# Kernel tuning notes

Hardware: AMD Instinct MI355X
Metric: run time of the kernel (lower is better)

Reference implementation:

```python
import jax, jax.numpy as jnp
import numpy as np

N_NODES = 50000
N_EDGES = 800000
IN_SIZE = 1024
EMB = 500


def setup_inputs() -> dict:
    key = jax.random.key(0)
    ks = jax.random.split(key, 9)
    x = jax.random.uniform(ks[0], (N_NODES, IN_SIZE), dtype=jnp.float32)
    edge_index = jax.random.randint(ks[1], (2, N_EDGES), 0, N_NODES, dtype=jnp.int32)
    edge_weight = jax.random.uniform(ks[2], (N_EDGES,), dtype=jnp.float32)
    s = 0.05
    wenc = jax.random.normal(ks[3], (EMB, IN_SIZE), dtype=jnp.float32) * s
    benc = jax.random.normal(ks[4], (EMB,), dtype=jnp.float32) * s
    wdec = jax.random.normal(ks[5], (IN_SIZE, EMB), dtype=jnp.float32) * s
    bdec = jax.random.normal(ks[6], (IN_SIZE,), dtype=jnp.float32) * s
    conv_weight = jax.random.normal(ks[7], (EMB, EMB), dtype=jnp.float32) * 0.1
    # lin.weight initialized N(0,0.1) + identity, per reset_parameters
    lin_weight = jax.random.normal(ks[8], (EMB, EMB), dtype=jnp.float32) * 0.1 + jnp.eye(EMB, dtype=jnp.float32)
    return {"x": x, "edge_index": edge_index, "edge_weight": edge_weight,
            "wenc": wenc, "benc": benc, "wdec": wdec, "bdec": bdec,
            "conv_weight": conv_weight, "lin_weight": lin_weight}


def reference(x, edge_index, edge_weight, wenc, benc, wdec, bdec, conv_weight, lin_weight):
    # encoder: h = sigmoid(x @ wenc^T + benc)          [N, EMB]
    h = jax.nn.sigmoid(x @ wenc.T + benc)
    # GraphConv (old PyG): neighbor transform then scatter-add to destinations
    h2 = h @ conv_weight                                # [N, EMB]
    src, dst = edge_index[0], edge_index[1]
    msgs = h2[src] * edge_weight[:, None]               # [E, EMB] gather + weight
    agg = jax.ops.segment_sum(msgs, dst, num_segments=x.shape[0])
    hout = agg + h @ lin_weight.T                       # root term via nn.Linear
    # decoder
    p = hout @ wdec.T + bdec                            # [N, IN_SIZE]
    return p
```

## Files before the change

### kernel.cpp

```cpp
#include <hip/hip_runtime.h>
#include <hip/hip_bf16.h>

typedef unsigned int u32;
typedef short bf16x8 __attribute__((ext_vector_type(8)));
typedef float floatx4 __attribute__((ext_vector_type(4)));

#define NNODES 50000
#define NEDGES 800000
#define INSZ   1024
#define EMB    500
#define EMBP   512

__device__ __forceinline__ short f2bf(float f) {
    u32 u = __builtin_bit_cast(u32, f);
    u32 r = u + 0x7FFFu + ((u >> 16) & 1u);
    return (short)(r >> 16);
}
__device__ __forceinline__ float bf2f(short h) {
    u32 u = ((u32)(unsigned short)h) << 16;
    return __builtin_bit_cast(float, u);
}

#define GLDS16(gp, lp) __builtin_amdgcn_global_load_lds( \
    (const __attribute__((address_space(1))) u32*)(gp),  \
    (__attribute__((address_space(3))) u32*)(lp), 16, 0, 0)

__global__ void pack_all(const float* __restrict__ wenc, const float* __restrict__ conv,
                         const float* __restrict__ lin,  const float* __restrict__ wdec,
                         short* __restrict__ wencP, short* __restrict__ Wmid,
                         short* __restrict__ wdecP) {
    int tid = blockIdx.x * 256 + threadIdx.x;
    {
        int m = tid >> 10, k = tid & 1023;
        wencP[tid] = (m < EMB) ? f2bf(wenc[m * INSZ + k]) : (short)0;
    }
    {
        int m = tid >> 10, k = tid & 1023;
        short v = 0;
        if (m < EMB) {
            if (k < EMBP) { if (k < EMB) v = f2bf(conv[k * EMB + m]); }
            else          { int kk = k - EMBP; if (kk < EMB) v = f2bf(lin[m * EMB + kk]); }
        }
        Wmid[tid] = v;
    }
    {
        int m = tid >> 9, k = tid & 511;
        wdecP[tid] = (k < EMB) ? f2bf(wdec[m * EMB + k]) : (short)0;
    }
}


__global__ __launch_bounds__(256)
void gemm_enc(const float* __restrict__ X, const short* __restrict__ Wp,
              const float* __restrict__ benc, short* __restrict__ H) {
    __shared__ short As[128 * 32];
    __shared__ short Bs[128 * 32];
    const int tid  = threadIdx.x;
    const int lane = tid & 63;
    const int wave = tid >> 6;
    const int wr   = (wave >> 1) * 64;
    const int wc   = (wave & 1) * 64;
    const int rowBase = blockIdx.y * 128;
    const int colBase = blockIdx.x * 128;

    floatx4 acc[4][4] = {};

    const int r0 = tid >> 2;
    const int c0 = (tid & 3) * 8;
    int ar0 = rowBase + r0;       if (ar0 >= NNODES) ar0 = NNODES - 1;
    int ar1 = rowBase + r0 + 64;  if (ar1 >= NNODES) ar1 = NNODES - 1;
    const float* xP0 = X + (size_t)ar0 * INSZ + c0;
    const float* xP1 = X + (size_t)ar1 * INSZ + c0;
    const short* bP0 = Wp + (size_t)(colBase + r0) * INSZ + c0;
    const short* bP1 = Wp + (size_t)(colBase + r0 + 64) * INSZ + c0;

    const int q8  = (lane >> 4) * 8;
    const int m16 = lane & 15;

    for (int k0 = 0; k0 < INSZ; k0 += 32) {
        {
            floatx4 fa = *(const floatx4*)(xP0 + k0);
            floatx4 fb = *(const floatx4*)(xP0 + k0 + 4);
            floatx4 fc = *(const floatx4*)(xP1 + k0);
            floatx4 fd = *(const floatx4*)(xP1 + k0 + 4);
            bf16x8 p0, p1;
#pragma unroll
            for (int j = 0; j < 4; ++j) {
                p0[j] = f2bf(fa[j]); p0[4 + j] = f2bf(fb[j]);
                p1[j] = f2bf(fc[j]); p1[4 + j] = f2bf(fd[j]);
            }
            *(bf16x8*)&As[tid * 8] = p0;
            *(bf16x8*)&As[2048 + tid * 8] = p1;
        }
        GLDS16(bP0 + k0, &Bs[tid * 8]);
        GLDS16(bP1 + k0, &Bs[2048 + tid * 8]);
        __syncthreads();

        bf16x8 af[4], bfr[4];
#pragma unroll
        for (int i = 0; i < 4; ++i) {
            af[i]  = *(const bf16x8*)&As[(wr + i * 16 + m16) * 32 + q8];
            bfr[i] = *(const bf16x8*)&Bs[(wc + i * 16 + m16) * 32 + q8];
        }
#pragma unroll
        for (int i = 0; i < 4; ++i)
#pragma unroll
            for (int j = 0; j < 4; ++j)
                acc[i][j] = __builtin_amdgcn_mfma_f32_16x16x32_bf16(af[i], bfr[j], acc[i][j], 0, 0, 0);
        __syncthreads();
    }

    const int rq = (lane >> 4) * 4;
#pragma unroll
    for (int i = 0; i < 4; ++i)
#pragma unroll
        for (int j = 0; j < 4; ++j)
#pragma unroll
            for (int reg = 0; reg < 4; ++reg) {
                int row = rowBase + wr + i * 16 + rq + reg;
                int col = colBase + wc + j * 16 + m16;
                if (row < NNODES) {
                    float b = (col < EMB) ? benc[col] : 0.f;
                    float v = 1.f / (1.f + __expf(-(acc[i][j][reg] + b)));
                    H[(size_t)row * EMBP + col] = f2bf(v);
                }
            }
}

__global__ __launch_bounds__(256)
void gemm_mid(const float* __restrict__ Agg, const short* __restrict__ H,
              const short* __restrict__ Wm, short* __restrict__ Hout) {
    __shared__ short As[128 * 32];
    __shared__ short Bs[128 * 32];
    const int tid  = threadIdx.x;
    const int lane = tid & 63;
    const int wave = tid >> 6;
    const int wr   = (wave >> 1) * 64;
    const int wc   = (wave & 1) * 64;
    const int rowBase = blockIdx.y * 128;
    const int colBase = blockIdx.x * 128;

    floatx4 acc[4][4] = {};

    const int r0 = tid >> 2;
    const int c0 = (tid & 3) * 8;
    int ar0 = rowBase + r0;       if (ar0 >= NNODES) ar0 = NNODES - 1;
    int ar1 = rowBase + r0 + 64;  if (ar1 >= NNODES) ar1 = NNODES - 1;
    const float* agP0 = Agg + (size_t)ar0 * EMBP + c0;
    const float* agP1 = Agg + (size_t)ar1 * EMBP + c0;
    const short* hP0  = H + (size_t)ar0 * EMBP + c0;
    const short* hP1  = H + (size_t)ar1 * EMBP + c0;
    const short* wP0  = Wm + (size_t)(colBase + r0) * 1024 + c0;
    const short* wP1  = Wm + (size_t)(colBase + r0 + 64) * 1024 + c0;

    const int q8  = (lane >> 4) * 8;
    const int m16 = lane & 15;

    for (int k0 = 0; k0 < 1024; k0 += 32) {
        if (k0 < 512) {
            floatx4 fa = *(const floatx4*)(agP0 + k0);
            floatx4 fb = *(const floatx4*)(agP0 + k0 + 4);
            floatx4 fc = *(const floatx4*)(agP1 + k0);
            floatx4 fd = *(const floatx4*)(agP1 + k0 + 4);
            bf16x8 p0, p1;
#pragma unroll
            for (int j = 0; j < 4; ++j) {
                p0[j] = f2bf(fa[j]); p0[4 + j] = f2bf(fb[j]);
                p1[j] = f2bf(fc[j]); p1[4 + j] = f2bf(fd[j]);
            }
            *(bf16x8*)&As[tid * 8] = p0;
            *(bf16x8*)&As[2048 + tid * 8] = p1;
        } else {
            GLDS16(hP0 + (k0 - 512), &As[tid * 8]);
            GLDS16(hP1 + (k0 - 512), &As[2048 + tid * 8]);
        }
        GLDS16(wP0 + k0, &Bs[tid * 8]);
        GLDS16(wP1 + k0, &Bs[2048 + tid * 8]);
        __syncthreads();

        bf16x8 af[4], bfr[4];
#pragma unroll
        for (int i = 0; i < 4; ++i) {
            af[i]  = *(const bf16x8*)&As[(wr + i * 16 + m16) * 32 + q8];
            bfr[i] = *(const bf16x8*)&Bs[(wc + i * 16 + m16) * 32 + q8];
        }
#pragma unroll
        for (int i = 0; i < 4; ++i)
#pragma unroll
            for (int j = 0; j < 4; ++j)
                acc[i][j] = __builtin_amdgcn_mfma_f32_16x16x32_bf16(af[i], bfr[j], acc[i][j], 0, 0, 0);
        __syncthreads();
    }

    const int rq = (lane >> 4) * 4;
#pragma unroll
    for (int i = 0; i < 4; ++i)
#pragma unroll
        for (int j = 0; j < 4; ++j)
#pragma unroll
            for (int reg = 0; reg < 4; ++reg) {
                int row = rowBase + wr + i * 16 + rq + reg;
                int col = colBase + wc + j * 16 + m16;
                if (row < NNODES)
                    Hout[(size_t)row * EMBP + col] = f2bf(acc[i][j][reg]);
            }
}

__global__ __launch_bounds__(256)
void gemm_dec(const short* __restrict__ Hout, const short* __restrict__ Wd,
              const float* __restrict__ bdec, float* __restrict__ Out) {
    __shared__ short As[128 * 32];
    __shared__ short Bs[128 * 32];
    const int tid  = threadIdx.x;
    const int lane = tid & 63;
    const int wave = tid >> 6;
    const int wr   = (wave >> 1) * 64;
    const int wc   = (wave & 1) * 64;
    const int rowBase = blockIdx.y * 128;
    const int colBase = blockIdx.x * 128;

    floatx4 acc[4][4] = {};

    const int r0 = tid >> 2;
    const int c0 = (tid & 3) * 8;
    int ar0 = rowBase + r0;       if (ar0 >= NNODES) ar0 = NNODES - 1;
    int ar1 = rowBase + r0 + 64;  if (ar1 >= NNODES) ar1 = NNODES - 1;
    const short* aP0 = Hout + (size_t)ar0 * EMBP + c0;
    const short* aP1 = Hout + (size_t)ar1 * EMBP + c0;
    const short* bP0 = Wd + (size_t)(colBase + r0) * EMBP + c0;
    const short* bP1 = Wd + (size_t)(colBase + r0 + 64) * EMBP + c0;

    const int q8  = (lane >> 4) * 8;
    const int m16 = lane & 15;

    for (int k0 = 0; k0 < EMBP; k0 += 32) {
        GLDS16(aP0 + k0, &As[tid * 8]);
        GLDS16(aP1 + k0, &As[2048 + tid * 8]);
        GLDS16(bP0 + k0, &Bs[tid * 8]);
        GLDS16(bP1 + k0, &Bs[2048 + tid * 8]);
        __syncthreads();

        bf16x8 af[4], bfr[4];
#pragma unroll
        for (int i = 0; i < 4; ++i) {
            af[i]  = *(const bf16x8*)&As[(wr + i * 16 + m16) * 32 + q8];
            bfr[i] = *(const bf16x8*)&Bs[(wc + i * 16 + m16) * 32 + q8];
        }
#pragma unroll
        for (int i = 0; i < 4; ++i)
#pragma unroll
            for (int j = 0; j < 4; ++j)
                acc[i][j] = __builtin_amdgcn_mfma_f32_16x16x32_bf16(af[i], bfr[j], acc[i][j], 0, 0, 0);
        __syncthreads();
    }

    const int rq = (lane >> 4) * 4;
#pragma unroll
    for (int i = 0; i < 4; ++i)
#pragma unroll
        for (int j = 0; j < 4; ++j)
#pragma unroll
            for (int reg = 0; reg < 4; ++reg) {
                int row = rowBase + wr + i * 16 + rq + reg;
                int col = colBase + wc + j * 16 + m16;
                if (row < NNODES)
                    Out[(size_t)row * INSZ + col] = acc[i][j][reg] + bdec[col];
            }
}


__global__ __launch_bounds__(256)
void count_edges(const int* __restrict__ dst, int* __restrict__ counts) {
    int e = blockIdx.x * 256 + threadIdx.x;
    atomicAdd(&counts[dst[e]], 1);
}

__global__ __launch_bounds__(1024)
void scan_counts(const int* __restrict__ counts, int* __restrict__ rowPtr,
                 int* __restrict__ cursor) {
    __shared__ int wsum[16];
    __shared__ int sbase;
    const int t = threadIdx.x;
    const int lane = t & 63;
    const int wv = t >> 6;
    if (t == 0) sbase = 0;
    for (int chunk = 0; chunk < 50176; chunk += 1024) {
        int i = chunk + t;
        int c = (i < NNODES) ? counts[i] : 0;
        int v = c;
#pragma unroll
        for (int off = 1; off < 64; off <<= 1) {
            int u = __shfl_up(v, off, 64);
            if (lane >= off) v += u;
        }
        if (lane == 63) wsum[wv] = v;
        __syncthreads();
        int woff = 0, total = 0;
#pragma unroll
        for (int w = 0; w < 16; ++w) {
            int s = wsum[w];
            if (w < wv) woff += s;
            total += s;
        }
        int base = sbase;
        __syncthreads();
        if (i < NNODES) {
            int p = base + woff + v - c;
            rowPtr[i] = p;
            cursor[i] = p;
        }
        if (t == 0) sbase = base + total;
        __syncthreads();
    }
}

__global__ __launch_bounds__(256)
void fill_csr(const int* __restrict__ src, const int* __restrict__ dst,
              const float* __restrict__ ew, int* __restrict__ cursor,
              int* __restrict__ csrSrc, float* __restrict__ csrW) {
    int e = blockIdx.x * 256 + threadIdx.x;
    int d = dst[e];
    int p = atomicAdd(&cursor[d], 1);
    csrSrc[p] = src[e];
    csrW[p]   = ew[e];
}

__global__ __launch_bounds__(256)
void aggregate(const short* __restrict__ H, const int* __restrict__ rowPtr,
               const int* __restrict__ counts, const int* __restrict__ csrSrc,
               const float* __restrict__ csrW, float* __restrict__ agg) {
    const int n    = blockIdx.x * 4 + (threadIdx.x >> 6);
    const int lane = threadIdx.x & 63;
    const int beg  = rowPtr[n];
    const int cnt  = counts[n];
    const short* hb = H + lane * 8;

    float acc[8] = {0.f, 0.f, 0.f, 0.f, 0.f, 0.f, 0.f, 0.f};
    int i = 0;
    for (; i + 2 <= cnt; i += 2) {
        int   s0 = csrSrc[beg + i];
        int   s1 = csrSrc[beg + i + 1];
        float w0 = csrW[beg + i];
        float w1 = csrW[beg + i + 1];
        bf16x8 v0 = *(const bf16x8*)(hb + (size_t)s0 * EMBP);
        bf16x8 v1 = *(const bf16x8*)(hb + (size_t)s1 * EMBP);
#pragma unroll
        for (int j = 0; j < 8; ++j)
            acc[j] += w0 * bf2f(v0[j]) + w1 * bf2f(v1[j]);
    }
    if (i < cnt) {
        int   s0 = csrSrc[beg + i];
        float w0 = csrW[beg + i];
        bf16x8 v0 = *(const bf16x8*)(hb + (size_t)s0 * EMBP);
#pragma unroll
        for (int j = 0; j < 8; ++j)
            acc[j] += w0 * bf2f(v0[j]);
    }

    floatx4 o0, o1;
#pragma unroll
    for (int j = 0; j < 4; ++j) { o0[j] = acc[j]; o1[j] = acc[4 + j]; }
    float* ap = agg + (size_t)n * EMBP + lane * 8;
    *(floatx4*)ap       = o0;
    *(floatx4*)(ap + 4) = o1;
}

extern "C" void kernel_launch(void* const* d_in, const int* in_sizes, int n_in,
                              void* d_out, int out_size, void* d_ws, size_t ws_size,
                              hipStream_t stream) {
    const float* x    = (const float*)d_in[0];
    const int*   ei   = (const int*)d_in[1];
    const float* ew   = (const float*)d_in[2];
    const float* wenc = (const float*)d_in[3];
    const float* benc = (const float*)d_in[4];
    const float* wdec = (const float*)d_in[5];
    const float* bdec = (const float*)d_in[6];
    const float* conv = (const float*)d_in[7];
    const float* lin  = (const float*)d_in[8];
    float* out = (float*)d_out;

    char* ws = (char*)d_ws;
    short* wencP = (short*)(ws);
    short* Wmid  = (short*)(ws + 1048576);
    short* wdecP = (short*)(ws + 2097152);
    short* h     = (short*)(ws + 3145728);
    short* hout  = (short*)(ws + 3145728 + 51200000);

    float* agg = (float*)d_out;

    char* scratch = (char*)d_out + 102400000;
    int*   counts = (int*)scratch;
    int*   rowPtr = counts + NNODES;
    int*   cursor = rowPtr + NNODES;
    int*   csrSrc = cursor + NNODES;
    float* csrW   = (float*)(csrSrc + NEDGES);

    hipMemsetAsync(counts, 0, (size_t)NNODES * 4, stream);

    dim3 blk(256);
    pack_all<<<2048, blk, 0, stream>>>(wenc, conv, lin, wdec, wencP, Wmid, wdecP);

    int rowTiles = (NNODES + 127) / 128;

    gemm_enc<<<dim3(EMBP / 128, rowTiles), blk, 0, stream>>>(x, wencP, benc, h);

    count_edges<<<NEDGES / 256, blk, 0, stream>>>(ei + NEDGES, counts);
    scan_counts<<<1, 1024, 0, stream>>>(counts, rowPtr, cursor);
    fill_csr<<<NEDGES / 256, blk, 0, stream>>>(ei, ei + NEDGES, ew, cursor, csrSrc, csrW);

    aggregate<<<NNODES / 4, blk, 0, stream>>>(h, rowPtr, counts, csrSrc, csrW, agg);

    gemm_mid<<<dim3(EMBP / 128, rowTiles), blk, 0, stream>>>(agg, h, Wmid, hout);

    gemm_dec<<<dim3(INSZ / 128, rowTiles), blk, 0, stream>>>(hout, wdecP, bdec, out);
}
```

Baseline: 957.8 us.

## Pre-convert X to bf16, double-buffer GEMMs, XCD swizzle, bf16 aggregation output

A separate kernel converts X to bf16 in scratch output memory, so the encoder GEMM can load A tiles asynchronously with global_load_lds. All three GEMMs now double-buffer LDS and prefetch the next K tile while computing the current one, and their block indices are remapped across XCDs. The aggregation is unrolled to four edges and writes bf16 instead of fp32, which halves its write traffic and lets gemm_mid load it directly. The trade-off is an extra full pass over X and reuse of the output buffer as scratch, with the counts memset moved after the encoder GEMM because that region is now overwritten.

```diff
diff --git a/kernel.cpp b/kernel.cpp
--- a/kernel.cpp
+++ b/kernel.cpp
@@ -24,6 +24,12 @@
 #define GLDS16(gp, lp) __builtin_amdgcn_global_load_lds( \
     (const __attribute__((address_space(1))) u32*)(gp),  \
     (__attribute__((address_space(3))) u32*)(lp), 16, 0, 0)
+
+__device__ __forceinline__ u32 xcd_swz(u32 orig, u32 q, u32 r) {
+    u32 xcd = orig & 7u, seq = orig >> 3;
+    u32 base = (xcd < r) ? xcd * (q + 1u) : r * (q + 1u) + (xcd - r) * q;
+    return base + seq;
+}
 
 __global__ void pack_all(const float* __restrict__ wenc, const float* __restrict__ conv,
                          const float* __restrict__ lin,  const float* __restrict__ wdec,
@@ -49,19 +55,31 @@
     }
 }
 
-
-__global__ __launch_bounds__(256)
-void gemm_enc(const float* __restrict__ X, const short* __restrict__ Wp,
+__global__ __launch_bounds__(256)
+void conv_x(const float* __restrict__ X, short* __restrict__ Xb) {
+    size_t base = ((size_t)blockIdx.x * 256 + threadIdx.x) * 8;
+    floatx4 f0 = *(const floatx4*)(X + base);
+    floatx4 f1 = *(const floatx4*)(X + base + 4);
+    bf16x8 p;
+#pragma unroll
+    for (int j = 0; j < 4; ++j) { p[j] = f2bf(f0[j]); p[4 + j] = f2bf(f1[j]); }
+    *(bf16x8*)(Xb + base) = p;
+}
+
+
+__global__ __launch_bounds__(256)
+void gemm_enc(const short* __restrict__ Xb, const short* __restrict__ Wp,
               const float* __restrict__ benc, short* __restrict__ H) {
-    __shared__ short As[128 * 32];
-    __shared__ short Bs[128 * 32];
+    __shared__ short As[2][128 * 32];
+    __shared__ short Bs[2][128 * 32];
     const int tid  = threadIdx.x;
     const int lane = tid & 63;
     const int wave = tid >> 6;
     const int wr   = (wave >> 1) * 64;
     const int wc   = (wave & 1) * 64;
-    const int rowBase = blockIdx.y * 128;
-    const int colBase = blockIdx.x * 128;
+    const u32 swz  = xcd_swz(blockIdx.y * 4 + blockIdx.x, 195, 4);
+    const int rowBase = (int)(swz >> 2) * 128;
+    const int colBase = (int)(swz & 3) * 128;
 
     floatx4 acc[4][4] = {};
 
@@ -69,38 +87,30 @@
     const int c0 = (tid & 3) * 8;
     int ar0 = rowBase + r0;       if (ar0 >= NNODES) ar0 = NNODES - 1;
     int ar1 = rowBase + r0 + 64;  if (ar1 >= NNODES) ar1 = NNODES - 1;
-    const float* xP0 = X + (size_t)ar0 * INSZ + c0;
-    const float* xP1 = X + (size_t)ar1 * INSZ + c0;
+    const short* aP0 = Xb + (size_t)ar0 * INSZ + c0;
+    const short* aP1 = Xb + (size_t)ar1 * INSZ + c0;
     const short* bP0 = Wp + (size_t)(colBase + r0) * INSZ + c0;
     const short* bP1 = Wp + (size_t)(colBase + r0 + 64) * INSZ + c0;
 
     const int q8  = (lane >> 4) * 8;
     const int m16 = lane & 15;
 
-    for (int k0 = 0; k0 < INSZ; k0 += 32) {
-        {
-            floatx4 fa = *(const floatx4*)(xP0 + k0);
-            floatx4 fb = *(const floatx4*)(xP0 + k0 + 4);
-            floatx4 fc = *(const floatx4*)(xP1 + k0);
-            floatx4 fd = *(const floatx4*)(xP1 + k0 + 4);
-            bf16x8 p0, p1;
-#pragma unroll
-            for (int j = 0; j < 4; ++j) {
-                p0[j] = f2bf(fa[j]); p0[4 + j] = f2bf(fb[j]);
-                p1[j] = f2bf(fc[j]); p1[4 + j] = f2bf(fd[j]);
-            }
-            *(bf16x8*)&As[tid * 8] = p0;
-            *(bf16x8*)&As[2048 + tid * 8] = p1;
-        }
-        GLDS16(bP0 + k0, &Bs[tid * 8]);
-        GLDS16(bP1 + k0, &Bs[2048 + tid * 8]);
-        __syncthreads();
-
+#define STAGE_E(buf, k0)                                   \
+    GLDS16(aP0 + (k0), &As[buf][tid * 8]);                 \
+    GLDS16(aP1 + (k0), &As[buf][2048 + tid * 8]);          \
+    GLDS16(bP0 + (k0), &Bs[buf][tid * 8]);                 \
+    GLDS16(bP1 + (k0), &Bs[buf][2048 + tid * 8]);
+
+    STAGE_E(0, 0);
+    __syncthreads();
+    int cur = 0;
+    for (int t = 0; t < 32; ++t) {
+        if (t + 1 < 32) { STAGE_E(cur ^ 1, (t + 1) * 32); }
         bf16x8 af[4], bfr[4];
 #pragma unroll
         for (int i = 0; i < 4; ++i) {
-            af[i]  = *(const bf16x8*)&As[(wr + i * 16 + m16) * 32 + q8];
-            bfr[i] = *(const bf16x8*)&Bs[(wc + i * 16 + m16) * 32 + q8];
+            af[i]  = *(const bf16x8*)&As[cur][(wr + i * 16 + m16) * 32 + q8];
+            bfr[i] = *(const bf16x8*)&Bs[cur][(wc + i * 16 + m16) * 32 + q8];
         }
 #pragma unroll
         for (int i = 0; i < 4; ++i)
@@ -108,7 +118,9 @@
             for (int j = 0; j < 4; ++j)
                 acc[i][j] = __builtin_amdgcn_mfma_f32_16x16x32_bf16(af[i], bfr[j], acc[i][j], 0, 0, 0);
         __syncthreads();
-    }
+        cur ^= 1;
+    }
+#undef STAGE_E
 
     const int rq = (lane >> 4) * 4;
 #pragma unroll
@@ -128,17 +140,18 @@
 }
 
 __global__ __launch_bounds__(256)
-void gemm_mid(const float* __restrict__ Agg, const short* __restrict__ H,
+void gemm_mid(const short* __restrict__ AggB, const short* __restrict__ H,
               const short* __restrict__ Wm, short* __restrict__ Hout) {
-    __shared__ short As[128 * 32];
-    __shared__ short Bs[128 * 32];
+    __shared__ short As[2][128 * 32];
+    __shared__ short Bs[2][128 * 32];
     const int tid  = threadIdx.x;
     const int lane = tid & 63;
     const int wave = tid >> 6;
     const int wr   = (wave >> 1) * 64;
     const int wc   = (wave & 1) * 64;
-    const int rowBase = blockIdx.y * 128;
-    const int colBase = blockIdx.x * 128;
+    const u32 swz  = xcd_swz(blockIdx.y * 4 + blockIdx.x, 195, 4);
+    const int rowBase = (int)(swz >> 2) * 128;
+    const int colBase = (int)(swz & 3) * 128;
 
     floatx4 acc[4][4] = {};
 
@@ -146,8 +159,8 @@
     const int c0 = (tid & 3) * 8;
     int ar0 = rowBase + r0;       if (ar0 >= NNODES) ar0 = NNODES - 1;
     int ar1 = rowBase + r0 + 64;  if (ar1 >= NNODES) ar1 = NNODES - 1;
-    const float* agP0 = Agg + (size_t)ar0 * EMBP + c0;
-    const float* agP1 = Agg + (size_t)ar1 * EMBP + c0;
+    const short* agP0 = AggB + (size_t)ar0 * EMBP + c0;
+    const short* agP1 = AggB + (size_t)ar1 * EMBP + c0;
     const short* hP0  = H + (size_t)ar0 * EMBP + c0;
     const short* hP1  = H + (size_t)ar1 * EMBP + c0;
     const short* wP0  = Wm + (size_t)(colBase + r0) * 1024 + c0;
@@ -156,33 +169,27 @@
     const int q8  = (lane >> 4) * 8;
     const int m16 = lane & 15;
 
-    for (int k0 = 0; k0 < 1024; k0 += 32) {
-        if (k0 < 512) {
-            floatx4 fa = *(const floatx4*)(agP0 + k0);
-            floatx4 fb = *(const floatx4*)(agP0 + k0 + 4);
-            floatx4 fc = *(const floatx4*)(agP1 + k0);
-            floatx4 fd = *(const floatx4*)(agP1 + k0 + 4);
-            bf16x8 p0, p1;
-#pragma unroll
-            for (int j = 0; j < 4; ++j) {
-                p0[j] = f2bf(fa[j]); p0[4 + j] = f2bf(fb[j]);
-                p1[j] = f2bf(fc[j]); p1[4 + j] = f2bf(fd[j]);
-            }
-            *(bf16x8*)&As[tid * 8] = p0;
-            *(bf16x8*)&As[2048 + tid * 8] = p1;
-        } else {
-            GLDS16(hP0 + (k0 - 512), &As[tid * 8]);
-            GLDS16(hP1 + (k0 - 512), &As[2048 + tid * 8]);
-        }
-        GLDS16(wP0 + k0, &Bs[tid * 8]);
-        GLDS16(wP1 + k0, &Bs[2048 + tid * 8]);
-        __syncthreads();
-
+#define STAGE_M(buf, k0)                                              \
+    if ((k0) < 512) {                                                 \
+        GLDS16(agP0 + (k0), &As[buf][tid * 8]);                       \
+        GLDS16(agP1 + (k0), &As[buf][2048 + tid * 8]);                \
+    } else {                                                          \
+        GLDS16(hP0 + ((k0) - 512), &As[buf][tid * 8]);                \
+        GLDS16(hP1 + ((k0) - 512), &As[buf][2048 + tid * 8]);         \
+    }                                                                 \
+    GLDS16(wP0 + (k0), &Bs[buf][tid * 8]);                            \
+    GLDS16(wP1 + (k0), &Bs[buf][2048 + tid * 8]);
+
+    STAGE_M(0, 0);
+    __syncthreads();
+    int cur = 0;
+    for (int t = 0; t < 32; ++t) {
+        if (t + 1 < 32) { STAGE_M(cur ^ 1, (t + 1) * 32); }
         bf16x8 af[4], bfr[4];
 #pragma unroll
         for (int i = 0; i < 4; ++i) {
-            af[i]  = *(const bf16x8*)&As[(wr + i * 16 + m16) * 32 + q8];
-            bfr[i] = *(const bf16x8*)&Bs[(wc + i * 16 + m16) * 32 + q8];
+            af[i]  = *(const bf16x8*)&As[cur][(wr + i * 16 + m16) * 32 + q8];
+            bfr[i] = *(const bf16x8*)&Bs[cur][(wc + i * 16 + m16) * 32 + q8];
         }
 #pragma unroll
         for (int i = 0; i < 4; ++i)
@@ -190,7 +197,9 @@
             for (int j = 0; j < 4; ++j)
                 acc[i][j] = __builtin_amdgcn_mfma_f32_16x16x32_bf16(af[i], bfr[j], acc[i][j], 0, 0, 0);
         __syncthreads();
-    }
+        cur ^= 1;
+    }
+#undef STAGE_M
 
     const int rq = (lane >> 4) * 4;
 #pragma unroll
@@ -209,15 +218,16 @@
 __global__ __launch_bounds__(256)
 void gemm_dec(const short* __restrict__ Hout, const short* __restrict__ Wd,
               const float* __restrict__ bdec, float* __restrict__ Out) {
-    __shared__ short As[128 * 32];
-    __shared__ short Bs[128 * 32];
+    __shared__ short As[2][128 * 32];
+    __shared__ short Bs[2][128 * 32];
     const int tid  = threadIdx.x;
     const int lane = tid & 63;
     const int wave = tid >> 6;
     const int wr   = (wave >> 1) * 64;
     const int wc   = (wave & 1) * 64;
-    const int rowBase = blockIdx.y * 128;
-    const int colBase = blockIdx.x * 128;
+    const u32 swz  = xcd_swz(blockIdx.y * 8 + blockIdx.x, 391, 0);
+    const int rowBase = (int)(swz >> 3) * 128;
+    const int colBase = (int)(swz & 7) * 128;
 
     floatx4 acc[4][4] = {};
 
@@ -233,18 +243,22 @@
     const int q8  = (lane >> 4) * 8;
     const int m16 = lane & 15;
 
-    for (int k0 = 0; k0 < EMBP; k0 += 32) {
-        GLDS16(aP0 + k0, &As[tid * 8]);
-        GLDS16(aP1 + k0, &As[2048 + tid * 8]);
-        GLDS16(bP0 + k0, &Bs[tid * 8]);
-        GLDS16(bP1 + k0, &Bs[2048 + tid * 8]);
-        __syncthreads();
-
+#define STAGE_D(buf, k0)                                   \
+    GLDS16(aP0 + (k0), &As[buf][tid * 8]);                 \
+    GLDS16(aP1 + (k0), &As[buf][2048 + tid * 8]);          \
+    GLDS16(bP0 + (k0), &Bs[buf][tid * 8]);                 \
+    GLDS16(bP1 + (k0), &Bs[buf][2048 + tid * 8]);
+
+    STAGE_D(0, 0);
+    __syncthreads();
+    int cur = 0;
+    for (int t = 0; t < 16; ++t) {
+        if (t + 1 < 16) { STAGE_D(cur ^ 1, (t + 1) * 32); }
         bf16x8 af[4], bfr[4];
 #pragma unroll
         for (int i = 0; i < 4; ++i) {
-            af[i]  = *(const bf16x8*)&As[(wr + i * 16 + m16) * 32 + q8];
-            bfr[i] = *(const bf16x8*)&Bs[(wc + i * 16 + m16) * 32 + q8];
+            af[i]  = *(const bf16x8*)&As[cur][(wr + i * 16 + m16) * 32 + q8];
+            bfr[i] = *(const bf16x8*)&Bs[cur][(wc + i * 16 + m16) * 32 + q8];
         }
 #pragma unroll
         for (int i = 0; i < 4; ++i)
@@ -252,7 +266,9 @@
             for (int j = 0; j < 4; ++j)
                 acc[i][j] = __builtin_amdgcn_mfma_f32_16x16x32_bf16(af[i], bfr[j], acc[i][j], 0, 0, 0);
         __syncthreads();
-    }
+        cur ^= 1;
+    }
+#undef STAGE_D
 
     const int rq = (lane >> 4) * 4;
 #pragma unroll
@@ -267,7 +283,6 @@
                     Out[(size_t)row * INSZ + col] = acc[i][j][reg] + bdec[col];
             }
 }
-
 
 __global__ __launch_bounds__(256)
 void count_edges(const int* __restrict__ dst, int* __restrict__ counts) {
@@ -328,7 +343,7 @@
 __global__ __launch_bounds__(256)
 void aggregate(const short* __restrict__ H, const int* __restrict__ rowPtr,
                const int* __restrict__ counts, const int* __restrict__ csrSrc,
-               const float* __restrict__ csrW, float* __restrict__ agg) {
+               const float* __restrict__ csrW, short* __restrict__ aggB) {
     const int n    = blockIdx.x * 4 + (threadIdx.x >> 6);
     const int lane = threadIdx.x & 63;
     const int beg  = rowPtr[n];
@@ -337,18 +352,21 @@
 
     float acc[8] = {0.f, 0.f, 0.f, 0.f, 0.f, 0.f, 0.f, 0.f};
     int i = 0;
-    for (; i + 2 <= cnt; i += 2) {
-        int   s0 = csrSrc[beg + i];
-        int   s1 = csrSrc[beg + i + 1];
-        float w0 = csrW[beg + i];
-        float w1 = csrW[beg + i + 1];
+    for (; i + 4 <= cnt; i += 4) {
+        int   s0 = csrSrc[beg + i],     s1 = csrSrc[beg + i + 1];
+        int   s2 = csrSrc[beg + i + 2], s3 = csrSrc[beg + i + 3];
+        float w0 = csrW[beg + i],       w1 = csrW[beg + i + 1];
+        float w2 = csrW[beg + i + 2],   w3 = csrW[beg + i + 3];
         bf16x8 v0 = *(const bf16x8*)(hb + (size_t)s0 * EMBP);
         bf16x8 v1 = *(const bf16x8*)(hb + (size_t)s1 * EMBP);
+        bf16x8 v2 = *(const bf16x8*)(hb + (size_t)s2 * EMBP);
+        bf16x8 v3 = *(const bf16x8*)(hb + (size_t)s3 * EMBP);
 #pragma unroll
         for (int j = 0; j < 8; ++j)
-            acc[j] += w0 * bf2f(v0[j]) + w1 * bf2f(v1[j]);
-    }
-    if (i < cnt) {
+            acc[j] += w0 * bf2f(v0[j]) + w1 * bf2f(v1[j])
+                    + w2 * bf2f(v2[j]) + w3 * bf2f(v3[j]);
+    }
+    for (; i < cnt; ++i) {
         int   s0 = csrSrc[beg + i];
         float w0 = csrW[beg + i];
         bf16x8 v0 = *(const bf16x8*)(hb + (size_t)s0 * EMBP);
@@ -357,12 +375,10 @@
             acc[j] += w0 * bf2f(v0[j]);
     }
 
-    floatx4 o0, o1;
-#pragma unroll
-    for (int j = 0; j < 4; ++j) { o0[j] = acc[j]; o1[j] = acc[4 + j]; }
-    float* ap = agg + (size_t)n * EMBP + lane * 8;
-    *(floatx4*)ap       = o0;
-    *(floatx4*)(ap + 4) = o1;
+    bf16x8 o;
+#pragma unroll
+    for (int j = 0; j < 8; ++j) o[j] = f2bf(acc[j]);
+    *(bf16x8*)(aggB + (size_t)n * EMBP + lane * 8) = o;
 }
 
 extern "C" void kernel_launch(void* const* d_in, const int* in_sizes, int n_in,
@@ -386,31 +402,30 @@
     short* h     = (short*)(ws + 3145728);
     short* hout  = (short*)(ws + 3145728 + 51200000);
 
-    float* agg = (float*)d_out;
-
-    char* scratch = (char*)d_out + 102400000;
+    short* aggB = (short*)d_out;
+    short* Xbf  = (short*)((char*)d_out + 102400000);
+    char*  scratch = (char*)d_out + 102400000;
     int*   counts = (int*)scratch;
     int*   rowPtr = counts + NNODES;
     int*   cursor = rowPtr + NNODES;
     int*   csrSrc = cursor + NNODES;
     float* csrW   = (float*)(csrSrc + NEDGES);
 
-    hipMemsetAsync(counts, 0, (size_t)NNODES * 4, stream);
-
     dim3 blk(256);
     pack_all<<<2048, blk, 0, stream>>>(wenc, conv, lin, wdec, wencP, Wmid, wdecP);
+    conv_x<<<25000, blk, 0, stream>>>(x, Xbf);
 
     int rowTiles = (NNODES + 127) / 128;
 
-    gemm_enc<<<dim3(EMBP / 128, rowTiles), blk, 0, stream>>>(x, wencP, benc, h);
-
+    gemm_enc<<<dim3(EMBP / 128, rowTiles), blk, 0, stream>>>(Xbf, wencP, benc, h);
+
+    hipMemsetAsync(counts, 0, (size_t)NNODES * 4, stream);
     count_edges<<<NEDGES / 256, blk, 0, stream>>>(ei + NEDGES, counts);
     scan_counts<<<1, 1024, 0, stream>>>(counts, rowPtr, cursor);
     fill_csr<<<NEDGES / 256, blk, 0, stream>>>(ei, ei + NEDGES, ew, cursor, csrSrc, csrW);
-
-    aggregate<<<NNODES / 4, blk, 0, stream>>>(h, rowPtr, counts, csrSrc, csrW, agg);
-
-    gemm_mid<<<dim3(EMBP / 128, rowTiles), blk, 0, stream>>>(agg, h, Wmid, hout);
+    aggregate<<<NNODES / 4, blk, 0, stream>>>(h, rowPtr, counts, csrSrc, csrW, aggB);
+
+    gemm_mid<<<dim3(EMBP / 128, rowTiles), blk, 0, stream>>>(aggB, h, Wmid, hout);
 
     gemm_dec<<<dim3(INSZ / 128, rowTiles), blk, 0, stream>>>(hout, wdecP, bdec, out);
 }
```

After: 930.1 us. 1.03x faster.
